# Performance work log

Measured on AMD Instinct MI355X. Metric: run time of the kernel, lower is better.

The kernel has to match this reference:

```python
import jax, jax.numpy as jnp
import numpy as np

HID, H, HKV, D, INT, S, T = 2048, 16, 8, 128, 6144, 4096, 512
POS = 0          # absolute position of the first token in this prefill chunk
EPS = 1e-6
SCALE = 1.0 / D ** 0.5
REP = H // HKV


def setup_inputs() -> dict:
    key = jax.random.key(0)
    ks = jax.random.split(key, 12)
    w = lambda k, sh: jax.random.normal(k, sh, dtype=jnp.float32) * 0.02

    hidden_conv = jax.random.normal(ks[0], (1, HID, 1, T), dtype=jnp.float32)

    # RoPE tables for absolute positions POS..POS+T-1, HF half-rotation layout
    inv_freq = 1.0 / (10000.0 ** (jnp.arange(0, D, 2, dtype=jnp.float32) / D))
    pos = (POS + jnp.arange(T, dtype=jnp.float32))
    ang = pos[:, None] * inv_freq[None, :]                      # (T, D/2)
    emb = jnp.concatenate([ang, ang], axis=-1)                  # (T, D)
    cos = jnp.cos(emb)[None]                                    # (1, T, D)
    sin = jnp.sin(emb)[None]

    # one-hot write mask: column t has a 1 at row POS+t
    update_mask = jnp.zeros((S, T), jnp.float32).at[POS + jnp.arange(T), jnp.arange(T)].set(1.0)[None, None]
    # causal mask over the cache: slot s visible to token t iff s <= POS+t
    attn_mask = jnp.where(jnp.arange(S)[None, :] <= (POS + jnp.arange(T))[:, None], 0.0, -1e4).astype(jnp.float32)[None, None]

    k_cache = jnp.zeros((1, HKV, S, D), jnp.float32)
    v_cache = jnp.zeros((1, HKV, S, D), jnp.float32)

    return dict(
        hidden_conv=hidden_conv, cos=cos, sin=sin,
        update_mask=update_mask, attn_mask=attn_mask,
        k_cache=k_cache, v_cache=v_cache,
        wq=w(ks[1], (H * D, HID)), wk=w(ks[2], (HKV * D, HID)),
        wv=w(ks[3], (HKV * D, HID)), wo=w(ks[4], (HID, H * D)),
        ln1_w=jnp.ones((HID,), jnp.float32), ln2_w=jnp.ones((HID,), jnp.float32),
        qn_w=jnp.ones((D,), jnp.float32), kn_w=jnp.ones((D,), jnp.float32),
        w_gate_up=w(ks[5], (2 * INT, HID)), w_down=w(ks[6], (HID, INT)),
    )


def _rms(x, w):
    return x * jax.lax.rsqrt(jnp.mean(x * x, axis=-1, keepdims=True) + EPS) * w


def _rotate_half(x):
    x1, x2 = jnp.split(x, 2, axis=-1)
    return jnp.concatenate([-x2, x1], axis=-1)


def reference(hidden_conv, cos, sin, update_mask, attn_mask, k_cache, v_cache,
              wq, wk, wv, wo, ln1_w, ln2_w, qn_w, kn_w, w_gate_up, w_down):
    # (1, HID, 1, T) conv layout -> (1, T, HID)
    x = jnp.transpose(hidden_conv[:, :, 0, :], (0, 2, 1))

    h = _rms(x, ln1_w)
    # 1x1 conv == linear; channel order h*D+d matches view(1,H,D,T)
    q = jnp.einsum('btc,oc->bto', h, wq).reshape(1, T, H, D).transpose(0, 2, 1, 3)    # (1,H,T,D)
    k = jnp.einsum('btc,oc->bto', h, wk).reshape(1, T, HKV, D).transpose(0, 2, 1, 3)  # (1,HKV,T,D)
    v = jnp.einsum('btc,oc->bto', h, wv).reshape(1, T, HKV, D).transpose(0, 2, 1, 3)

    q = _rms(q, qn_w)
    k = _rms(k, kn_w)

    cos_b = cos[:, None]  # (1,1,T,D)
    sin_b = sin[:, None]
    q = q * cos_b + _rotate_half(q) * sin_b
    k = k * cos_b + _rotate_half(k) * sin_b

    # matmul-based KV cache write via one-hot mask (faithful to original)
    k_inc = jnp.matmul(update_mask, k)                 # (1,HKV,S,D)
    v_inc = jnp.matmul(update_mask, v)
    write_any = jnp.sum(update_mask, axis=-1, keepdims=True)  # (1,1,S,1)
    k_full = k_cache * (1.0 - write_any) + k_inc
    v_full = v_cache * (1.0 - write_any) + v_inc

    k_rep = jnp.repeat(k_full, REP, axis=1)            # (1,H,S,D)
    v_rep = jnp.repeat(v_full, REP, axis=1)

    scores = jnp.einsum('bhtd,bhsd->bhts', q, k_rep) * SCALE + attn_mask  # (1,H,T,S)
    attn = jax.nn.softmax(scores, axis=-1)
    out = jnp.einsum('bhts,bhsd->bhtd', attn, v_rep)   # (1,H,T,D)

    o_in = out.transpose(0, 2, 1, 3).reshape(1, T, H * D)
    attn_out = jnp.einsum('btc,oc->bto', o_in, wo)
    hidden = x + attn_out

    h2 = _rms(hidden, ln2_w)
    gate_up = jnp.einsum('btc,oc->bto', h2, w_gate_up)
    gate, up = jnp.split(gate_up, 2, axis=-1)
    mlp = jnp.einsum('bti,oi->bto', jax.nn.silu(gate) * up, w_down)
    hidden = hidden + mlp

    hidden_out = jnp.transpose(hidden, (0, 2, 1))[:, :, None, :]  # back to (1,HID,1,T)
    return hidden_out, k_full, v_full


if __name__ == '__main__':
    outs = reference(**setup_inputs())
    print([o.shape for o in outs])
```

## Files before the change

kernel.cpp:

```cpp
#include <hip/hip_runtime.h>
#include <hip/hip_bf16.h>
#include <hip/hip_fp16.h>

#define TT 512
#define HIDD 2048
#define NH 16
#define NKV 8
#define DD 128
#define INTR 6144
#define SEQ 4096
#define SCALE 0.08838834764831845f

typedef __attribute__((ext_vector_type(8))) short short8;
typedef __attribute__((ext_vector_type(4))) float floatx4;

static __device__ __forceinline__ unsigned short f2b(float f) {
  unsigned int u = __float_as_uint(f);
  u += 0x7fffu + ((u >> 16) & 1u);
  return (unsigned short)(u >> 16);
}

static __device__ __forceinline__ unsigned int f2b2(float a, float b) {
  __hip_bfloat162 h = __float22bfloat162_rn(make_float2(a, b));
  return *reinterpret_cast<unsigned int*>(&h);
}


static __device__ __forceinline__ void gld16(const void* g, void* l) {
  __builtin_amdgcn_global_load_lds(
      (const __attribute__((address_space(1))) unsigned int*)g,
      (__attribute__((address_space(3))) unsigned int*)l, 16, 0, 0);
}

template <int BM, bool B16>
static __device__ __forceinline__ void stage_tile(const unsigned short* __restrict__ A, int lda,
                                                  const void* __restrict__ B, int ldb, int k0,
                                                  unsigned char* buf, int wave, int lane) {
  {
    const int rpw = BM >> 2;
    const int rl = lane >> 2;
    const int c8 = (lane & 3) << 3;
#pragma unroll
    for (int i = 0; i < BM / 64; ++i) {
      const int rbase = wave * rpw + i * 16;
      gld16(A + (size_t)(rbase + rl) * lda + k0 + c8, buf + (size_t)rbase * 64);
    }
  }
  unsigned char* Bb = buf + BM * 64;
  if constexpr (B16) {
    const unsigned short* Bh = (const unsigned short*)B;
    const int rl = lane >> 2;
    const int c8 = (lane & 3) << 3;
#pragma unroll
    for (int i = 0; i < 2; ++i) {
      const int rbase = wave * 32 + i * 16;
      gld16(Bh + (size_t)(rbase + rl) * ldb + k0 + c8, Bb + (size_t)rbase * 64);
    }
  } else {
    const float* Bf = (const float*)B;
    const int rl = lane >> 3;
    const int sp = lane & 7;
#pragma unroll
    for (int i = 0; i < 4; ++i) {
      const int rbase = wave * 32 + i * 8;
      const int r = rbase + rl;
      gld16(Bf + (size_t)r * ldb + k0 + ((sp ^ (r & 7)) << 2), Bb + (size_t)rbase * 128);
    }
  }
}

template <int BM, bool B16>
static __device__ __forceinline__ void frags_from(const unsigned char* buf, int wr, int wc,
                                                  int lrow, int koff,
                                                  short8 (&af)[BM / 32], short8 (&bfr)[4]) {
  const unsigned short* Ab = (const unsigned short*)buf;
#pragma unroll
  for (int mi = 0; mi < BM / 32; ++mi)
    af[mi] = *reinterpret_cast<const short8*>(Ab + (size_t)(wr + mi * 16 + lrow) * 32 + koff);
  if constexpr (B16) {
    const unsigned short* Bb = (const unsigned short*)(buf + BM * 64);
#pragma unroll
    for (int ni = 0; ni < 4; ++ni)
      bfr[ni] = *reinterpret_cast<const short8*>(Bb + (size_t)(wc + ni * 16 + lrow) * 32 + koff);
  } else {
    const float* Bf = (const float*)(buf + BM * 64);
    const int s0 = koff >> 2;
#pragma unroll
    for (int ni = 0; ni < 4; ++ni) {
      const int r = wc + ni * 16 + lrow;
      const float4 x = *reinterpret_cast<const float4*>(Bf + (size_t)r * 32 + ((s0 ^ (r & 7)) << 2));
      const float4 y = *reinterpret_cast<const float4*>(Bf + (size_t)r * 32 + (((s0 + 1) ^ (r & 7)) << 2));
      union { short8 s; unsigned int u[4]; } pk;
      pk.u[0] = f2b2(x.x, x.y); pk.u[1] = f2b2(x.z, x.w);
      pk.u[2] = f2b2(y.x, y.y); pk.u[3] = f2b2(y.z, y.w);
      bfr[ni] = pk.s;
    }
  }
}

template <int BM, bool B16>
static __device__ __forceinline__ void gemm_core(const unsigned short* __restrict__ A, int lda,
                                                 const void* __restrict__ B, int ldb,
                                                 int kbeg, int kend, floatx4 (&acc)[BM / 32][4],
                                                 unsigned char* Ls) {
  constexpr int MI = BM / 32;
  constexpr int TILE = BM * 64 + (B16 ? 8192 : 16384);
  constexpr int NB = (BM / 64) + (B16 ? 2 : 4);
  const int tid = threadIdx.x;
  const int lane = tid & 63, wave = tid >> 6;
  const int wr = (wave >> 1) * (BM >> 1);
  const int wc = (wave & 1) << 6;
  const int lrow = lane & 15;
  const int koff = (lane >> 4) << 3;
  const int NT = (kend - kbeg) >> 5;
  stage_tile<BM, B16>(A, lda, B, ldb, kbeg,      Ls,        wave, lane);
  stage_tile<BM, B16>(A, lda, B, ldb, kbeg + 32, Ls + TILE, wave, lane);
  int p = 0;
  for (int t = 0; t < NT - 1; ++t) {
    if constexpr (NB == 6)      asm volatile("s_waitcnt vmcnt(6)" ::: "memory");
    else if constexpr (NB == 3) asm volatile("s_waitcnt vmcnt(3)" ::: "memory");
    else if constexpr (NB == 4) asm volatile("s_waitcnt vmcnt(4)" ::: "memory");
    else                        asm volatile("s_waitcnt vmcnt(5)" ::: "memory");
    __builtin_amdgcn_sched_barrier(0);
    __builtin_amdgcn_s_barrier();
    short8 af[MI], bfr[4];
    frags_from<BM, B16>(Ls + p * TILE, wr, wc, lrow, koff, af, bfr);
    asm volatile("s_waitcnt lgkmcnt(0)" ::: "memory");
    __builtin_amdgcn_sched_barrier(0);
    __builtin_amdgcn_s_barrier();
    if (t + 2 < NT)
      stage_tile<BM, B16>(A, lda, B, ldb, kbeg + (t + 2) * 32, Ls + p * TILE, wave, lane);
#pragma unroll
    for (int mi = 0; mi < MI; ++mi)
#pragma unroll
      for (int ni = 0; ni < 4; ++ni)
        acc[mi][ni] = __builtin_amdgcn_mfma_f32_16x16x32_bf16(af[mi], bfr[ni], acc[mi][ni], 0, 0, 0);
    p ^= 1;
  }
  asm volatile("s_waitcnt vmcnt(0)" ::: "memory");
  __builtin_amdgcn_sched_barrier(0);
  __builtin_amdgcn_s_barrier();
  {
    short8 af[MI], bfr[4];
    frags_from<BM, B16>(Ls + p * TILE, wr, wc, lrow, koff, af, bfr);
#pragma unroll
    for (int mi = 0; mi < MI; ++mi)
#pragma unroll
      for (int ni = 0; ni < 4; ++ni)
        acc[mi][ni] = __builtin_amdgcn_mfma_f32_16x16x32_bf16(af[mi], bfr[ni], acc[mi][ni], 0, 0, 0);
  }
}

#define EPI_VARS \
  const int lane = threadIdx.x & 63; \
  const int wave = threadIdx.x >> 6; \
  const int wc = (wave & 1) << 6;    \
  const int lrow = lane & 15;        \
  const int quad = lane >> 4;

#define ZERO_ACC(MI_) \
  floatx4 acc[MI_][4]; \
  _Pragma("unroll") for (int mi = 0; mi < MI_; ++mi) \
  _Pragma("unroll") for (int ni = 0; ni < 4; ++ni) { floatx4 z = {0.f, 0.f, 0.f, 0.f}; acc[mi][ni] = z; }

template <int S>
static __device__ __forceinline__ void swz(int b, int& mt, int& nt, int& s) {
  mt = (b >> 3) & 3;
  const int gid = ((b >> 5) << 3) | (b & 7);
  nt = gid / S;
  s = gid - nt * S;
}


__global__ __launch_bounds__(1024) void k_rms1(const float* __restrict__ conv,
                                               const float* __restrict__ w,
                                               float* __restrict__ xb,
                                               unsigned short* __restrict__ h1b) {
  const int t0 = blockIdx.x << 5;
  const int tid = threadIdx.x;
  const int j = tid & 31;
  const int g = tid >> 5;
  __shared__ float part[32][32];
  __shared__ float tile[32][33];
  __shared__ float rs[32];
  float ss = 0.f;
  for (int c0 = 0; c0 < HIDD; c0 += 32) {
    const float v = conv[(size_t)(c0 + g) * TT + t0 + j];
    ss += v * v;
  }
  part[g][j] = ss;
  __syncthreads();
  if (g == 0) {
    float tot = 0.f;
#pragma unroll
    for (int q = 0; q < 32; ++q) tot += part[q][j];
    rs[j] = rsqrtf(tot * (1.0f / HIDD) + 1e-6f);
  }
  __syncthreads();
  for (int c0 = 0; c0 < HIDD; c0 += 32) {
    tile[g][j] = conv[(size_t)(c0 + g) * TT + t0 + j];
    __syncthreads();
    const float v = tile[j][g];
    const float rv = rs[g];
    xb[(size_t)(t0 + g) * HIDD + c0 + j] = v;
    h1b[(size_t)(t0 + g) * HIDD + c0 + j] = f2b(v * rv * w[c0 + j]);
    __syncthreads();
  }
}

__global__ __launch_bounds__(256) void k_gemm_qkv(const unsigned short* __restrict__ h1b,
                                                  const float* __restrict__ wq,
                                                  const float* __restrict__ wk,
                                                  const float* __restrict__ wv,
                                                  float* __restrict__ Pq) {
  __shared__ __align__(16) unsigned char Ls[2 * (128 * 64 + 16384)];
  int mt, nt, s;
  swz<4>(blockIdx.x, mt, nt, s);
  const int m0 = mt << 7, n0 = nt << 7;
  const float* Bp;
  if (n0 < 2048)      Bp = wq + (size_t)n0 * HIDD;
  else if (n0 < 3072) Bp = wk + (size_t)(n0 - 2048) * HIDD;
  else                Bp = wv + (size_t)(n0 - 3072) * HIDD;
  ZERO_ACC(4)
  gemm_core<128, false>(h1b + (size_t)m0 * HIDD, HIDD, Bp, HIDD, s * 512, s * 512 + 512, acc, Ls);
  EPI_VARS
  const int wr = (wave >> 1) << 6;
  float* out = Pq + (size_t)s * (TT * 4096);
#pragma unroll
  for (int mi = 0; mi < 4; ++mi)
#pragma unroll
    for (int ni = 0; ni < 4; ++ni)
#pragma unroll
      for (int rr = 0; rr < 4; ++rr) {
        const int row = m0 + wr + mi * 16 + quad * 4 + rr;
        const int col = n0 + wc + ni * 16 + lrow;
        out[(size_t)row * 4096 + col] = acc[mi][ni][rr];
      }
}

__global__ __launch_bounds__(128) void k_rope(const float* __restrict__ Pq,
                                              const float* __restrict__ cosb,
                                              const float* __restrict__ sinb,
                                              const float* __restrict__ qnw,
                                              const float* __restrict__ knw,
                                              unsigned short* __restrict__ qb,
                                              unsigned short* __restrict__ kb,
                                              unsigned short* __restrict__ vtb,
                                              float* __restrict__ kout,
                                              float* __restrict__ vout) {
  const int u = blockIdx.x;
  const int t = blockIdx.y;
  const int d = threadIdx.x;
  __shared__ float red[2];
  __shared__ float sh[DD];
  int slot;
  if (u < NH)            slot = u * DD + d;
  else if (u < NH + NKV) slot = 2048 + (u - NH) * DD + d;
  else                   slot = 3072 + (u - NH - NKV) * DD + d;
  const size_t idx = (size_t)t * 4096 + slot;
  float val = Pq[idx] + Pq[idx + TT * 4096] + Pq[idx + 2 * TT * 4096] + Pq[idx + 3 * TT * 4096];
  if (u < NH + NKV) {
    float ss = val * val;
    const int lane = d & 63, wid = d >> 6;
#pragma unroll
    for (int o = 32; o; o >>= 1) ss += __shfl_xor(ss, o);
    if (!lane) red[wid] = ss;
    __syncthreads();
    const float r = rsqrtf((red[0] + red[1]) * (1.0f / DD) + 1e-6f);
    const float w = (u < NH) ? qnw[d] : knw[d];
    const float nv = val * r * w;
    sh[d] = nv;
    __syncthreads();
    const float partner = sh[d ^ 64];
    const float rh = (d < 64) ? -partner : partner;
    const float o = nv * cosb[(size_t)t * DD + d] + rh * sinb[(size_t)t * DD + d];
    if (u < NH) {
      qb[(size_t)u * TT * DD + (size_t)t * DD + d] = f2b(o);
    } else {
      const int kh = u - NH;
      kout[(size_t)kh * SEQ * DD + (size_t)t * DD + d] = o;
      kb[(size_t)kh * TT * DD + (size_t)t * DD + d] = f2b(o);
    }
  } else {
    const int vh = u - NH - NKV;
    vout[(size_t)vh * SEQ * DD + (size_t)t * DD + d] = val;
    vtb[(size_t)vh * DD * TT + (size_t)d * TT + t] = f2b(val);
  }
}

__global__ __launch_bounds__(256) void k_tail(const float* __restrict__ kc,
                                              const float* __restrict__ vc,
                                              float* __restrict__ ko,
                                              float* __restrict__ vo) {
  const int i = blockIdx.x * 256 + threadIdx.x;
  const int e = i << 2;
  const int s = (e >> 7) & (SEQ - 1);
  if (s >= TT) {
    reinterpret_cast<float4*>(ko)[i] = reinterpret_cast<const float4*>(kc)[i];
    reinterpret_cast<float4*>(vo)[i] = reinterpret_cast<const float4*>(vc)[i];
  }
}

__global__ __launch_bounds__(256) void k_scores(const unsigned short* __restrict__ qb,
                                                const unsigned short* __restrict__ kb,
                                                float* __restrict__ sc) {
  __shared__ __align__(16) unsigned char Ls[2 * (64 * 64 + 8192)];
  const int m0 = blockIdx.x << 6, n0 = blockIdx.y << 7, h = blockIdx.z;
  ZERO_ACC(2)
  gemm_core<64, true>(qb + (size_t)h * TT * DD + (size_t)m0 * DD, DD,
                      kb + (size_t)(h >> 1) * TT * DD + (size_t)n0 * DD, DD, 0, DD, acc, Ls);
  EPI_VARS
  const int wr = (wave >> 1) << 5;
  float* out = sc + (size_t)h * TT * TT;
#pragma unroll
  for (int mi = 0; mi < 2; ++mi)
#pragma unroll
    for (int ni = 0; ni < 4; ++ni)
#pragma unroll
      for (int rr = 0; rr < 4; ++rr) {
        const int t = m0 + wr + mi * 16 + quad * 4 + rr;
        const int s = n0 + wc + ni * 16 + lrow;
        float v = acc[mi][ni][rr] * SCALE;
        if (s > t) v += -10000.0f;
        out[(size_t)t * TT + s] = v;
      }
}

__global__ __launch_bounds__(256) void k_softmax(const float* __restrict__ sc,
                                                 unsigned short* __restrict__ Pb) {
  const int h = blockIdx.x >> 9, t = blockIdx.x & 511;
  const int tid = threadIdx.x;
  const float* row = sc + ((size_t)h * TT + t) * TT;
  float v0 = row[tid], v1 = row[tid + 256];
  __shared__ float red[4];
  const int lane = tid & 63, wid = tid >> 6;
  float m = fmaxf(v0, v1);
#pragma unroll
  for (int o = 32; o; o >>= 1) m = fmaxf(m, __shfl_xor(m, o));
  if (!lane) red[wid] = m;
  __syncthreads();
  m = fmaxf(fmaxf(red[0], red[1]), fmaxf(red[2], red[3]));
  const float e0 = __expf(v0 - m), e1 = __expf(v1 - m);
  float s = e0 + e1;
  __syncthreads();
#pragma unroll
  for (int o = 32; o; o >>= 1) s += __shfl_xor(s, o);
  if (!lane) red[wid] = s;
  __syncthreads();
  const float inv = 1.0f / (red[0] + red[1] + red[2] + red[3]);
  unsigned short* orow = Pb + ((size_t)h * TT + t) * TT;
  orow[tid] = f2b(e0 * inv);
  orow[tid + 256] = f2b(e1 * inv);
}

__global__ __launch_bounds__(256) void k_pv(const unsigned short* __restrict__ Pb,
                                            const unsigned short* __restrict__ vtb,
                                            float* __restrict__ Ppv) {
  __shared__ __align__(16) unsigned char Ls[2 * (64 * 64 + 8192)];
  const int m0 = blockIdx.x << 6, h = blockIdx.y, s = blockIdx.z;
  ZERO_ACC(2)
  gemm_core<64, true>(Pb + (size_t)h * TT * TT + (size_t)m0 * TT, TT,
                      vtb + (size_t)(h >> 1) * DD * TT, TT, s * 128, s * 128 + 128, acc, Ls);
  EPI_VARS
  const int wr = (wave >> 1) << 5;
  float* out = Ppv + (size_t)s * (TT * HIDD);
#pragma unroll
  for (int mi = 0; mi < 2; ++mi)
#pragma unroll
    for (int ni = 0; ni < 4; ++ni)
#pragma unroll
      for (int rr = 0; rr < 4; ++rr) {
        const int row = m0 + wr + mi * 16 + quad * 4 + rr;
        const int col = wc + ni * 16 + lrow;
        out[(size_t)row * HIDD + h * DD + col] = acc[mi][ni][rr];
      }
}

__global__ __launch_bounds__(256) void k_red_pv(const float* __restrict__ Ppv,
                                                unsigned short* __restrict__ o_inb) {
  const int i = blockIdx.x * 256 + threadIdx.x;
  const float4* p = reinterpret_cast<const float4*>(Ppv);
  float4 a = p[i];
  const float4 b = p[i + 262144], c = p[i + 524288], d = p[i + 786432];
  a.x += b.x + c.x + d.x; a.y += b.y + c.y + d.y;
  a.z += b.z + c.z + d.z; a.w += b.w + c.w + d.w;
  uint2 o;
  o.x = f2b2(a.x, a.y);
  o.y = f2b2(a.z, a.w);
  *reinterpret_cast<uint2*>(o_inb + (size_t)i * 4) = o;
}

__global__ __launch_bounds__(256) void k_gemm_o(const unsigned short* __restrict__ o_inb,
                                                const float* __restrict__ wo,
                                                float* __restrict__ Po) {
  __shared__ __align__(16) unsigned char Ls[2 * (128 * 64 + 16384)];
  int mt, nt, s;
  swz<8>(blockIdx.x, mt, nt, s);
  const int m0 = mt << 7, n0 = nt << 7;
  ZERO_ACC(4)
  gemm_core<128, false>(o_inb + (size_t)m0 * HIDD, HIDD, wo + (size_t)n0 * HIDD, HIDD,
                        s * 256, s * 256 + 256, acc, Ls);
  EPI_VARS
  const int wr = (wave >> 1) << 6;
  float* out = Po + (size_t)s * (TT * HIDD);
#pragma unroll
  for (int mi = 0; mi < 4; ++mi)
#pragma unroll
    for (int ni = 0; ni < 4; ++ni)
#pragma unroll
      for (int rr = 0; rr < 4; ++rr) {
        const int row = m0 + wr + mi * 16 + quad * 4 + rr;
        const int col = n0 + wc + ni * 16 + lrow;
        out[(size_t)row * HIDD + col] = acc[mi][ni][rr];
      }
}

__global__ __launch_bounds__(256) void k_rms2(const float* __restrict__ xb,
                                              const float* __restrict__ Po,
                                              const float* __restrict__ w,
                                              float* __restrict__ hidden,
                                              unsigned short* __restrict__ h2b) {
  const int t = blockIdx.x;
  const int tid = threadIdx.x;
  float2 v[4];
  float ss = 0.f;
#pragma unroll
  for (int i = 0; i < 4; ++i) {
    const int c = (tid << 1) + (i << 9);
    const size_t idx = (size_t)t * HIDD + c;
    float2 a = *reinterpret_cast<const float2*>(xb + idx);
#pragma unroll
    for (int sp = 0; sp < 8; ++sp) {
      const float2 b = *reinterpret_cast<const float2*>(Po + idx + (size_t)sp * (TT * HIDD));
      a.x += b.x; a.y += b.y;
    }
    v[i] = a;
    ss += a.x * a.x + a.y * a.y;
  }
  __shared__ float red[4];
  const int lane = tid & 63, wid = tid >> 6;
#pragma unroll
  for (int o = 32; o; o >>= 1) ss += __shfl_xor(ss, o);
  if (!lane) red[wid] = ss;
  __syncthreads();
  const float tot = red[0] + red[1] + red[2] + red[3];
  const float r = rsqrtf(tot * (1.0f / HIDD) + 1e-6f);
#pragma unroll
  for (int i = 0; i < 4; ++i) {
    const int c = (tid << 1) + (i << 9);
    const size_t idx = (size_t)t * HIDD + c;
    *reinterpret_cast<float2*>(hidden + idx) = v[i];
    const float2 wv2 = *reinterpret_cast<const float2*>(w + c);
    *reinterpret_cast<unsigned int*>(h2b + idx) = f2b2(v[i].x * r * wv2.x, v[i].y * r * wv2.y);
  }
}

__global__ __launch_bounds__(256) void k_gemm_gu(const unsigned short* __restrict__ h2b,
                                                 const float* __restrict__ wgu,
                                                 __half* __restrict__ guh) {
  __shared__ __align__(16) unsigned char Ls[2 * (128 * 64 + 16384)];
  int mt, nt, s;
  swz<2>(blockIdx.x, mt, nt, s);
  const int m0 = mt << 7, n0 = nt << 7;
  ZERO_ACC(4)
  gemm_core<128, false>(h2b + (size_t)m0 * HIDD, HIDD, wgu + (size_t)n0 * HIDD, HIDD,
                        s * 1024, s * 1024 + 1024, acc, Ls);
  EPI_VARS
  const int wr = (wave >> 1) << 6;
  __half* out = guh + (size_t)s * (TT * 2 * INTR);
#pragma unroll
  for (int mi = 0; mi < 4; ++mi)
#pragma unroll
    for (int ni = 0; ni < 4; ++ni)
#pragma unroll
      for (int rr = 0; rr < 4; ++rr) {
        const int row = m0 + wr + mi * 16 + quad * 4 + rr;
        const int col = n0 + wc + ni * 16 + lrow;
        out[(size_t)row * (2 * INTR) + col] = __float2half(acc[mi][ni][rr]);
      }
}

__global__ __launch_bounds__(256) void k_silu(const __half* __restrict__ guh,
                                              unsigned short* __restrict__ actb) {
  const int j0 = (blockIdx.x * 256 + threadIdx.x) << 1;
  const int t = blockIdx.y;
  const size_t base = (size_t)t * (2 * INTR) + j0;
  const size_t off = (size_t)TT * (2 * INTR);
  const float2 g0 = __half22float2(*reinterpret_cast<const __half2*>(guh + base));
  const float2 g1 = __half22float2(*reinterpret_cast<const __half2*>(guh + off + base));
  const float2 u0 = __half22float2(*reinterpret_cast<const __half2*>(guh + base + INTR));
  const float2 u1 = __half22float2(*reinterpret_cast<const __half2*>(guh + off + base + INTR));
  const float gx = g0.x + g1.x, gy = g0.y + g1.y;
  const float ux = u0.x + u1.x, uy = u0.y + u1.y;
  const float a0 = gx / (1.f + __expf(-gx)) * ux;
  const float a1 = gy / (1.f + __expf(-gy)) * uy;
  *reinterpret_cast<unsigned int*>(actb + (size_t)t * INTR + j0) = f2b2(a0, a1);
}

__global__ __launch_bounds__(256) void k_gemm_down(const unsigned short* __restrict__ actb,
                                                   const float* __restrict__ wdn,
                                                   float* __restrict__ Pdn) {
  __shared__ __align__(16) unsigned char Ls[2 * (128 * 64 + 16384)];
  int mt, nt, s;
  swz<8>(blockIdx.x, mt, nt, s);
  const int m0 = mt << 7, n0 = nt << 7;
  ZERO_ACC(4)
  gemm_core<128, false>(actb + (size_t)m0 * INTR, INTR, wdn + (size_t)n0 * INTR, INTR,
                        s * 768, s * 768 + 768, acc, Ls);
  EPI_VARS
  const int wr = (wave >> 1) << 6;
  float* out = Pdn + (size_t)s * (TT * HIDD);
#pragma unroll
  for (int mi = 0; mi < 4; ++mi)
#pragma unroll
    for (int ni = 0; ni < 4; ++ni)
#pragma unroll
      for (int rr = 0; rr < 4; ++rr) {
        const int row = m0 + wr + mi * 16 + quad * 4 + rr;
        const int col = n0 + wc + ni * 16 + lrow;
        out[(size_t)row * HIDD + col] = acc[mi][ni][rr];
      }
}

__global__ __launch_bounds__(256) void k_final(const float* __restrict__ hidden,
                                               const float* __restrict__ Pdn,
                                               float* __restrict__ out0) {
  __shared__ float tile[32][33];
  const int c0 = blockIdx.x << 5, t0 = blockIdx.y << 5;
  const int tx = threadIdx.x & 31, ty0 = (threadIdx.x >> 5) << 2;
#pragma unroll
  for (int i = 0; i < 4; ++i) {
    const int t = t0 + ty0 + i;
    const size_t idx = (size_t)t * HIDD + c0 + tx;
    float a = hidden[idx];
#pragma unroll
    for (int sp = 0; sp < 8; ++sp) a += Pdn[idx + (size_t)sp * (TT * HIDD)];
    tile[ty0 + i][tx] = a;
  }
  __syncthreads();
#pragma unroll
  for (int i = 0; i < 4; ++i)
    out0[(size_t)(c0 + ty0 + i) * TT + t0 + tx] = tile[tx][ty0 + i];
}

extern "C" void kernel_launch(void* const* d_in, const int* in_sizes, int n_in,
                              void* d_out, int out_size, void* d_ws, size_t ws_size,
                              hipStream_t stream) {
  const float* conv   = (const float*)d_in[0];
  const float* cosb   = (const float*)d_in[1];
  const float* sinb   = (const float*)d_in[2];
  const float* kcache = (const float*)d_in[5];
  const float* vcache = (const float*)d_in[6];
  const float* wq  = (const float*)d_in[7];
  const float* wk  = (const float*)d_in[8];
  const float* wv  = (const float*)d_in[9];
  const float* wo  = (const float*)d_in[10];
  const float* ln1 = (const float*)d_in[11];
  const float* ln2 = (const float*)d_in[12];
  const float* qnw = (const float*)d_in[13];
  const float* knw = (const float*)d_in[14];
  const float* wgu = (const float*)d_in[15];
  const float* wdn = (const float*)d_in[16];

  float* ws = (float*)d_ws;
  float* xb = ws + 0;
  unsigned short* h1b  = (unsigned short*)(ws + 1048576);
  unsigned short* o_inb = h1b;
  unsigned short* h2b  = (unsigned short*)(ws + 1572864);
  float* hidden = ws + 2097152;
  unsigned short* qb  = (unsigned short*)(ws + 3145728);
  unsigned short* kb  = qb + 1048576;
  unsigned short* vtb = kb + 524288;
  unsigned short* actb = (unsigned short*)(ws + 4194304);
  float* R   = ws + 5767168;
  float* Pq  = R;
  unsigned short* Pb = (unsigned short*)R;
  float* sc  = R + 2097152;
  float* Ppv = R + 2097152;
  float* Po  = R;
  __half* guh = (__half*)R;
  float* Pdn = R;

  float* out0 = (float*)d_out;
  float* kout = out0 + 1048576;
  float* vout = kout + 4194304;

  k_rms1<<<16, 1024, 0, stream>>>(conv, ln1, xb, h1b);
  k_gemm_qkv<<<512, 256, 0, stream>>>(h1b, wq, wk, wv, Pq);
  k_rope<<<dim3(NH + 2 * NKV, TT), 128, 0, stream>>>(Pq, cosb, sinb, qnw, knw, qb, kb, vtb, kout, vout);
  k_tail<<<4096, 256, 0, stream>>>(kcache, vcache, kout, vout);
  k_scores<<<dim3(8, 4, NH), 256, 0, stream>>>(qb, kb, sc);
  k_softmax<<<NH * TT, 256, 0, stream>>>(sc, Pb);
  k_pv<<<dim3(8, NH, 4), 256, 0, stream>>>(Pb, vtb, Ppv);
  k_red_pv<<<1024, 256, 0, stream>>>(Ppv, o_inb);
  k_gemm_o<<<512, 256, 0, stream>>>(o_inb, wo, Po);
  k_rms2<<<TT, 256, 0, stream>>>(xb, Po, ln2, hidden, h2b);
  k_gemm_gu<<<768, 256, 0, stream>>>(h2b, wgu, guh);
  k_silu<<<dim3(12, TT), 256, 0, stream>>>(guh, actb);
  k_gemm_down<<<512, 256, 0, stream>>>(actb, wdn, Pdn);
  k_final<<<dim3(HIDD / 32, TT / 32), 256, 0, stream>>>(hidden, Pdn, out0);
}
```

Baseline: 465.4 us.

## Swizzle LDS bf16 tiles, store split-K partials in fp16, deepen split-K

XOR-swizzles the 16-byte column chunks of the bf16 A/B tiles in shared memory so that fragment reads spread across banks and avoid conflicts. The split-K partial sums of the QKV, O and down projections are now written and reduced as fp16 instead of fp32, halving partial-buffer traffic. The O and down GEMMs also use more K splits (16 and 12), which gives more blocks for parallelism. In exchange, partials lose precision and the reductions read more slices.

```diff
diff --git a/kernel.cpp b/kernel.cpp
--- a/kernel.cpp
+++ b/kernel.cpp
@@ -39,7 +39,7 @@
   {
     const int rpw = BM >> 2;
     const int rl = lane >> 2;
-    const int c8 = (lane & 3) << 3;
+    const int c8 = (((lane & 3) ^ ((rl >> 1) & 3)) << 3);
 #pragma unroll
     for (int i = 0; i < BM / 64; ++i) {
       const int rbase = wave * rpw + i * 16;
@@ -50,7 +50,7 @@
   if constexpr (B16) {
     const unsigned short* Bh = (const unsigned short*)B;
     const int rl = lane >> 2;
-    const int c8 = (lane & 3) << 3;
+    const int c8 = (((lane & 3) ^ ((rl >> 1) & 3)) << 3);
 #pragma unroll
     for (int i = 0; i < 2; ++i) {
       const int rbase = wave * 32 + i * 16;
@@ -71,20 +71,21 @@
 
 template <int BM, bool B16>
 static __device__ __forceinline__ void frags_from(const unsigned char* buf, int wr, int wc,
-                                                  int lrow, int koff,
+                                                  int lrow, int q,
                                                   short8 (&af)[BM / 32], short8 (&bfr)[4]) {
+  const int koffA = ((q ^ ((lrow >> 1) & 3)) << 3);
   const unsigned short* Ab = (const unsigned short*)buf;
 #pragma unroll
   for (int mi = 0; mi < BM / 32; ++mi)
-    af[mi] = *reinterpret_cast<const short8*>(Ab + (size_t)(wr + mi * 16 + lrow) * 32 + koff);
+    af[mi] = *reinterpret_cast<const short8*>(Ab + (size_t)(wr + mi * 16 + lrow) * 32 + koffA);
   if constexpr (B16) {
     const unsigned short* Bb = (const unsigned short*)(buf + BM * 64);
 #pragma unroll
     for (int ni = 0; ni < 4; ++ni)
-      bfr[ni] = *reinterpret_cast<const short8*>(Bb + (size_t)(wc + ni * 16 + lrow) * 32 + koff);
+      bfr[ni] = *reinterpret_cast<const short8*>(Bb + (size_t)(wc + ni * 16 + lrow) * 32 + koffA);
   } else {
     const float* Bf = (const float*)(buf + BM * 64);
-    const int s0 = koff >> 2;
+    const int s0 = q << 1;
 #pragma unroll
     for (int ni = 0; ni < 4; ++ni) {
       const int r = wc + ni * 16 + lrow;
@@ -111,7 +112,7 @@
   const int wr = (wave >> 1) * (BM >> 1);
   const int wc = (wave & 1) << 6;
   const int lrow = lane & 15;
-  const int koff = (lane >> 4) << 3;
+  const int q = lane >> 4;
   const int NT = (kend - kbeg) >> 5;
   stage_tile<BM, B16>(A, lda, B, ldb, kbeg,      Ls,        wave, lane);
   stage_tile<BM, B16>(A, lda, B, ldb, kbeg + 32, Ls + TILE, wave, lane);
@@ -124,7 +125,7 @@
     __builtin_amdgcn_sched_barrier(0);
     __builtin_amdgcn_s_barrier();
     short8 af[MI], bfr[4];
-    frags_from<BM, B16>(Ls + p * TILE, wr, wc, lrow, koff, af, bfr);
+    frags_from<BM, B16>(Ls + p * TILE, wr, wc, lrow, q, af, bfr);
     asm volatile("s_waitcnt lgkmcnt(0)" ::: "memory");
     __builtin_amdgcn_sched_barrier(0);
     __builtin_amdgcn_s_barrier();
@@ -142,7 +143,7 @@
   __builtin_amdgcn_s_barrier();
   {
     short8 af[MI], bfr[4];
-    frags_from<BM, B16>(Ls + p * TILE, wr, wc, lrow, koff, af, bfr);
+    frags_from<BM, B16>(Ls + p * TILE, wr, wc, lrow, q, af, bfr);
 #pragma unroll
     for (int mi = 0; mi < MI; ++mi)
 #pragma unroll
@@ -212,7 +213,7 @@
                                                   const float* __restrict__ wq,
                                                   const float* __restrict__ wk,
                                                   const float* __restrict__ wv,
-                                                  float* __restrict__ Pq) {
+                                                  __half* __restrict__ Pq) {
   __shared__ __align__(16) unsigned char Ls[2 * (128 * 64 + 16384)];
   int mt, nt, s;
   swz<4>(blockIdx.x, mt, nt, s);
@@ -225,7 +226,7 @@
   gemm_core<128, false>(h1b + (size_t)m0 * HIDD, HIDD, Bp, HIDD, s * 512, s * 512 + 512, acc, Ls);
   EPI_VARS
   const int wr = (wave >> 1) << 6;
-  float* out = Pq + (size_t)s * (TT * 4096);
+  __half* out = Pq + (size_t)s * (TT * 4096);
 #pragma unroll
   for (int mi = 0; mi < 4; ++mi)
 #pragma unroll
@@ -234,11 +235,11 @@
       for (int rr = 0; rr < 4; ++rr) {
         const int row = m0 + wr + mi * 16 + quad * 4 + rr;
         const int col = n0 + wc + ni * 16 + lrow;
-        out[(size_t)row * 4096 + col] = acc[mi][ni][rr];
+        out[(size_t)row * 4096 + col] = __float2half(acc[mi][ni][rr]);
       }
 }
 
-__global__ __launch_bounds__(128) void k_rope(const float* __restrict__ Pq,
+__global__ __launch_bounds__(128) void k_rope(const __half* __restrict__ Pq,
                                               const float* __restrict__ cosb,
                                               const float* __restrict__ sinb,
                                               const float* __restrict__ qnw,
@@ -258,7 +259,8 @@
   else if (u < NH + NKV) slot = 2048 + (u - NH) * DD + d;
   else                   slot = 3072 + (u - NH - NKV) * DD + d;
   const size_t idx = (size_t)t * 4096 + slot;
-  float val = Pq[idx] + Pq[idx + TT * 4096] + Pq[idx + 2 * TT * 4096] + Pq[idx + 3 * TT * 4096];
+  float val = __half2float(Pq[idx]) + __half2float(Pq[idx + (size_t)TT * 4096]) +
+              __half2float(Pq[idx + 2 * (size_t)TT * 4096]) + __half2float(Pq[idx + 3 * (size_t)TT * 4096]);
   if (u < NH + NKV) {
     float ss = val * val;
     const int lane = d & 63, wid = d >> 6;
@@ -392,17 +394,17 @@
 
 __global__ __launch_bounds__(256) void k_gemm_o(const unsigned short* __restrict__ o_inb,
                                                 const float* __restrict__ wo,
-                                                float* __restrict__ Po) {
+                                                __half* __restrict__ Po) {
   __shared__ __align__(16) unsigned char Ls[2 * (128 * 64 + 16384)];
   int mt, nt, s;
-  swz<8>(blockIdx.x, mt, nt, s);
+  swz<16>(blockIdx.x, mt, nt, s);
   const int m0 = mt << 7, n0 = nt << 7;
   ZERO_ACC(4)
   gemm_core<128, false>(o_inb + (size_t)m0 * HIDD, HIDD, wo + (size_t)n0 * HIDD, HIDD,
-                        s * 256, s * 256 + 256, acc, Ls);
+                        s * 128, s * 128 + 128, acc, Ls);
   EPI_VARS
   const int wr = (wave >> 1) << 6;
-  float* out = Po + (size_t)s * (TT * HIDD);
+  __half* out = Po + (size_t)s * (TT * HIDD);
 #pragma unroll
   for (int mi = 0; mi < 4; ++mi)
 #pragma unroll
@@ -411,12 +413,12 @@
       for (int rr = 0; rr < 4; ++rr) {
         const int row = m0 + wr + mi * 16 + quad * 4 + rr;
         const int col = n0 + wc + ni * 16 + lrow;
-        out[(size_t)row * HIDD + col] = acc[mi][ni][rr];
+        out[(size_t)row * HIDD + col] = __float2half(acc[mi][ni][rr]);
       }
 }
 
 __global__ __launch_bounds__(256) void k_rms2(const float* __restrict__ xb,
-                                              const float* __restrict__ Po,
+                                              const __half* __restrict__ Po,
                                               const float* __restrict__ w,
                                               float* __restrict__ hidden,
                                               unsigned short* __restrict__ h2b) {
@@ -430,8 +432,8 @@
     const size_t idx = (size_t)t * HIDD + c;
     float2 a = *reinterpret_cast<const float2*>(xb + idx);
 #pragma unroll
-    for (int sp = 0; sp < 8; ++sp) {
-      const float2 b = *reinterpret_cast<const float2*>(Po + idx + (size_t)sp * (TT * HIDD));
+    for (int sp = 0; sp < 16; ++sp) {
+      const float2 b = __half22float2(*reinterpret_cast<const __half2*>(Po + idx + (size_t)sp * (TT * HIDD)));
       a.x += b.x; a.y += b.y;
     }
     v[i] = a;
@@ -499,17 +501,17 @@
 
 __global__ __launch_bounds__(256) void k_gemm_down(const unsigned short* __restrict__ actb,
                                                    const float* __restrict__ wdn,
-                                                   float* __restrict__ Pdn) {
+                                                   __half* __restrict__ Pdn) {
   __shared__ __align__(16) unsigned char Ls[2 * (128 * 64 + 16384)];
   int mt, nt, s;
-  swz<8>(blockIdx.x, mt, nt, s);
+  swz<12>(blockIdx.x, mt, nt, s);
   const int m0 = mt << 7, n0 = nt << 7;
   ZERO_ACC(4)
   gemm_core<128, false>(actb + (size_t)m0 * INTR, INTR, wdn + (size_t)n0 * INTR, INTR,
-                        s * 768, s * 768 + 768, acc, Ls);
+                        s * 512, s * 512 + 512, acc, Ls);
   EPI_VARS
   const int wr = (wave >> 1) << 6;
-  float* out = Pdn + (size_t)s * (TT * HIDD);
+  __half* out = Pdn + (size_t)s * (TT * HIDD);
 #pragma unroll
   for (int mi = 0; mi < 4; ++mi)
 #pragma unroll
@@ -518,12 +520,12 @@
       for (int rr = 0; rr < 4; ++rr) {
         const int row = m0 + wr + mi * 16 + quad * 4 + rr;
         const int col = n0 + wc + ni * 16 + lrow;
-        out[(size_t)row * HIDD + col] = acc[mi][ni][rr];
+        out[(size_t)row * HIDD + col] = __float2half(acc[mi][ni][rr]);
       }
 }
 
 __global__ __launch_bounds__(256) void k_final(const float* __restrict__ hidden,
-                                               const float* __restrict__ Pdn,
+                                               const __half* __restrict__ Pdn,
                                                float* __restrict__ out0) {
   __shared__ float tile[32][33];
   const int c0 = blockIdx.x << 5, t0 = blockIdx.y << 5;
@@ -534,7 +536,7 @@
     const size_t idx = (size_t)t * HIDD + c0 + tx;
     float a = hidden[idx];
 #pragma unroll
-    for (int sp = 0; sp < 8; ++sp) a += Pdn[idx + (size_t)sp * (TT * HIDD)];
+    for (int sp = 0; sp < 12; ++sp) a += __half2float(Pdn[idx + (size_t)sp * (TT * HIDD)]);
     tile[ty0 + i][tx] = a;
   }
   __syncthreads();
@@ -573,30 +575,30 @@
   unsigned short* vtb = kb + 524288;
   unsigned short* actb = (unsigned short*)(ws + 4194304);
   float* R   = ws + 5767168;
-  float* Pq  = R;
+  __half* Pqh = (__half*)R;
   unsigned short* Pb = (unsigned short*)R;
   float* sc  = R + 2097152;
   float* Ppv = R + 2097152;
-  float* Po  = R;
+  __half* Poh = (__half*)R;
   __half* guh = (__half*)R;
-  float* Pdn = R;
+  __half* Pdnh = (__half*)R;
 
   float* out0 = (float*)d_out;
   float* kout = out0 + 1048576;
   float* vout = kout + 4194304;
 
   k_rms1<<<16, 1024, 0, stream>>>(conv, ln1, xb, h1b);
-  k_gemm_qkv<<<512, 256, 0, stream>>>(h1b, wq, wk, wv, Pq);
-  k_rope<<<dim3(NH + 2 * NKV, TT), 128, 0, stream>>>(Pq, cosb, sinb, qnw, knw, qb, kb, vtb, kout, vout);
+  k_gemm_qkv<<<512, 256, 0, stream>>>(h1b, wq, wk, wv, Pqh);
+  k_rope<<<dim3(NH + 2 * NKV, TT), 128, 0, stream>>>(Pqh, cosb, sinb, qnw, knw, qb, kb, vtb, kout, vout);
   k_tail<<<4096, 256, 0, stream>>>(kcache, vcache, kout, vout);
   k_scores<<<dim3(8, 4, NH), 256, 0, stream>>>(qb, kb, sc);
   k_softmax<<<NH * TT, 256, 0, stream>>>(sc, Pb);
   k_pv<<<dim3(8, NH, 4), 256, 0, stream>>>(Pb, vtb, Ppv);
   k_red_pv<<<1024, 256, 0, stream>>>(Ppv, o_inb);
-  k_gemm_o<<<512, 256, 0, stream>>>(o_inb, wo, Po);
-  k_rms2<<<TT, 256, 0, stream>>>(xb, Po, ln2, hidden, h2b);
+  k_gemm_o<<<1024, 256, 0, stream>>>(o_inb, wo, Poh);
+  k_rms2<<<TT, 256, 0, stream>>>(xb, Poh, ln2, hidden, h2b);
   k_gemm_gu<<<768, 256, 0, stream>>>(h2b, wgu, guh);
   k_silu<<<dim3(12, TT), 256, 0, stream>>>(guh, actb);
-  k_gemm_down<<<512, 256, 0, stream>>>(actb, wdn, Pdn);
-  k_final<<<dim3(HIDD / 32, TT / 32), 256, 0, stream>>>(hidden, Pdn, out0);
-}
+  k_gemm_down<<<768, 256, 0, stream>>>(actb, wdn, Pdnh);
+  k_final<<<dim3(HIDD / 32, TT / 32), 256, 0, stream>>>(hidden, Pdnh, out0);
+}
```

Measured after the change: 470.7 us. Within noise of the previous version (+1.1%).
